# Performance work log

Measured on AMD Instinct MI355X. Metric: run time of the kernel, lower is better.

## Reference

```python
import jax, jax.numpy as jnp
import numpy as np

N = 50000   # nodes
F = 128     # v_feats
K = 128     # filters
H = 3       # multi_head
M = 10      # fixed neighbor count (hardcoded repeat(1,10,1) in source)


def setup_inputs() -> dict:
    key = jax.random.key(0)
    ks = jax.random.split(key, 10)
    vertices = jax.random.normal(ks[0], (N, F), jnp.float32)
    nh_indices = jax.random.randint(ks[1], (N, M), 0, N)
    int_indices = jax.random.randint(ks[2], (N, M), 0, N)
    nh_edges = jax.random.uniform(ks[3], (N, M), jnp.float32)
    int_edges = jax.random.uniform(ks[4], (N, M), jnp.float32)
    is_int = jax.random.randint(ks[5], (N,), 0, 2)
    scale = 0.05
    Wvc = jax.random.normal(ks[6], (H, F, K), jnp.float32) * scale
    Wvn_int = jax.random.normal(ks[7], (H, F, K), jnp.float32) * scale
    Wvn_nh = jax.random.normal(ks[8], (H, F, K), jnp.float32) * scale
    a = jax.random.normal(ks[9], (H, 2 * K, 1), jnp.float32) * scale
    bv = jnp.zeros((H, K), jnp.float32)
    return dict(vertices=vertices, nh_indices=nh_indices, int_indices=int_indices,
                nh_edges=nh_edges, int_edges=int_edges, is_int=is_int,
                Wvc=Wvc, bv=bv, Wvn_int=Wvn_int, Wvn_nh=Wvn_nh, a=a)


def reference(vertices, nh_indices, int_indices, nh_edges, int_edges, is_int,
              Wvc, bv, Wvn_int, Wvn_nh, a):
    n = vertices.shape[0]
    k = a.shape[1] // 2
    # Project center and neighbor features for all heads at once.
    Zc = jnp.einsum('nf,hfk->hnk', vertices, Wvc)        # [H,N,K]
    Vint = jnp.einsum('nf,hfk->hnk', vertices, Wvn_int)  # [H,N,K]
    Vnh = jnp.einsum('nf,hfk->hnk', vertices, Wvn_nh)    # [H,N,K]
    # cat((neighbor, center)) @ a  ==  neighbor @ a[:k] + center @ a[k:]
    a_n = a[:, :k, 0]  # [H,K]
    a_c = a[:, k:, 0]  # [H,K]
    e_center = jnp.einsum('hnk,hk->hn', Zc, a_c)[:, :, None]  # [H,N,1]

    def branch(Vside, idx, edges):
        mask = (idx != -1).astype(vertices.dtype)           # [N,M], -1 = pad
        g = Vside[:, idx]                                   # [H,N,M,K] gather
        e = jnp.einsum('hnmk,hk->hnm', g, a_n) + e_center   # [H,N,M]
        # faithful to source: scores zeroed (not -inf) by mask/edges before softmax
        e = e * mask[None] * edges[None]
        alpha = jax.nn.softmax(e, axis=2)                   # [H,N,M]
        norm = jnp.maximum(mask.sum(axis=1), 1.0)           # [N]
        Zn = jnp.einsum('hnmk,hnm->hnk', g * mask[None, :, :, None], alpha)
        return Zn / norm[None, :, None]

    Zn_inter = branch(Vint, int_indices, int_edges)
    Zn_chain = branch(Vnh, nh_indices, nh_edges)
    z = jax.nn.relu(Zc + Zn_inter + Zn_chain + bv[:, None, :])  # [H,N,K]
    # torch.cat(head outputs, dim=1) -> [N, H*K]
    return jnp.transpose(z, (1, 0, 2)).reshape(n, -1)
```

## Files before the change

kernel.cpp:

```cpp
#include <hip/hip_runtime.h>
#include <stdint.h>

#define N_V 50000
#define F_DIM 128
#define K_DIM 128
#define H_DIM 3
#define M_DIM 10

using bf16x8 = __attribute__((ext_vector_type(8))) short;
using f32x4  = __attribute__((ext_vector_type(4))) float;

__device__ inline unsigned short f2bf(float f) {
    union { float f; uint32_t u; } v; v.f = f;
    uint32_t u = v.u;
    u += 0x7fffu + ((u >> 16) & 1u);
    return (unsigned short)(u >> 16);
}

#define LDS_AS __attribute__((address_space(3)))
__device__ inline void gl2lds16(const void* g, void* l) {
    __builtin_amdgcn_global_load_lds(
        (const __attribute__((address_space(1))) unsigned int*)g,
        (LDS_AS unsigned int*)l, 16, 0, 0);
}

#define WTOT (9 * 128 * 128)
#define XCH  (N_V * 16)
#define WACT (9 * 128)

__global__ void prep(const float* __restrict__ Wvc,
                     const float* __restrict__ Wvn_int,
                     const float* __restrict__ Wvn_nh,
                     const float* __restrict__ X,
                     const float* __restrict__ a,
                     unsigned short* __restrict__ Wt,
                     unsigned short* __restrict__ Xb,
                     unsigned short* __restrict__ wab) {
    int idx = blockIdx.x * 256 + threadIdx.x;
    if (idx < WTOT) {
        int b   = idx >> 14;
        int rem = idx & 16383;
        int k = rem >> 7;
        int f = rem & 127;
        int h = b / 3, t = b - 3 * h;
        const float* src = (t == 0) ? Wvc : (t == 1) ? Wvn_int : Wvn_nh;
        Wt[idx] = f2bf(src[(h * 128 + f) * 128 + k]);
        return;
    }
    int xi = idx - WTOT;
    if (xi < XCH) {
        const float4* Xv = (const float4*)X;
        float4 v0 = Xv[xi * 2];
        float4 v1 = Xv[xi * 2 + 1];
        uint4 o;
        o.x = (uint32_t)f2bf(v0.x) | ((uint32_t)f2bf(v0.y) << 16);
        o.y = (uint32_t)f2bf(v0.z) | ((uint32_t)f2bf(v0.w) << 16);
        o.z = (uint32_t)f2bf(v1.x) | ((uint32_t)f2bf(v1.y) << 16);
        o.w = (uint32_t)f2bf(v1.z) | ((uint32_t)f2bf(v1.w) << 16);
        *(uint4*)&Xb[(size_t)xi * 8] = o;
        return;
    }
    int wi = xi - XCH;
    if (wi < WACT) {
        int b = wi >> 7, f = wi & 127;
        int h = b / 3, t = b - 3 * h;
        const float* src = (t == 0) ? Wvc : (t == 1) ? Wvn_int : Wvn_nh;
        const float4* wrow = (const float4*)&src[(h * 128 + f) * 128];
        const float4* av   = (const float4*)&a[h * 256 + (t == 0 ? 128 : 0)];
        float acc = 0.f;
        #pragma unroll 8
        for (int c = 0; c < 32; ++c) {
            float4 w = wrow[c], x = av[c];
            acc += w.x * x.x + w.y * x.y + w.z * x.z + w.w * x.w;
        }
        wab[b * 128 + f] = f2bf(acc);
    }
}

__global__ __launch_bounds__(256, 3) void gemm_kernel(
    const unsigned short* __restrict__ Xb,
    const unsigned short* __restrict__ Wt,
    const unsigned short* __restrict__ wab,
    float* __restrict__ out,
    uint8_t* __restrict__ Vint,
    uint8_t* __restrict__ Vnh,
    float* __restrict__ e_center,
    float* __restrict__ e_int,
    float* __restrict__ e_nh) {
    __shared__ unsigned short As[64 * 128];

    const int tid    = threadIdx.x;
    const int b      = blockIdx.y;
    const int h      = b / 3;
    const int t      = b - 3 * h;
    const int m_base = blockIdx.x * 64;
    const int wv     = tid >> 6;
    const int lane   = tid & 63;
    const int q      = lane >> 4;
    const int ln     = lane & 15;
    const int cb     = (wv >> 1) * 64;
    const int rb     = (wv & 1) * 32;

    const unsigned short* Wb = Wt + b * 16384;
    bf16x8 bfr[4][4];
    #pragma unroll
    for (int ct = 0; ct < 4; ++ct) {
        int col = cb + 4 * ln + ct;
        #pragma unroll
        for (int kk = 0; kk < 4; ++kk)
            bfr[ct][kk] = *(const bf16x8*)&Wb[col * 128 + kk * 32 + q * 8];
    }

    #pragma unroll
    for (int it = 0; it < 4; ++it) {
        int c16 = it * 256 + tid;
        int r   = c16 >> 4;
        int p   = c16 & 15;
        int lch = p ^ (r & 15);
        int gr  = m_base + r;
        if (gr >= N_V) gr = 0;
        gl2lds16(Xb + (size_t)gr * 128 + lch * 8, &As[c16 * 8]);
    }
    __syncthreads();

    bf16x8 afr[2][4];
    #pragma unroll
    for (int rt = 0; rt < 2; ++rt) {
        int r = rb + rt * 16 + ln;
        #pragma unroll
        for (int kk = 0; kk < 4; ++kk) {
            int p = (kk * 4 + q) ^ ln;
            afr[rt][kk] = *(const bf16x8*)&As[r * 128 + p * 8];
        }
    }

    f32x4 acc[2][4];
    #pragma unroll
    for (int rt = 0; rt < 2; ++rt)
        #pragma unroll
        for (int ct = 0; ct < 4; ++ct) acc[rt][ct] = (f32x4){0.f, 0.f, 0.f, 0.f};

    #pragma unroll
    for (int rt = 0; rt < 2; ++rt)
        #pragma unroll
        for (int kk = 0; kk < 4; ++kk)
            #pragma unroll
            for (int ct = 0; ct < 4; ++ct)
                acc[rt][ct] = __builtin_amdgcn_mfma_f32_16x16x32_bf16(
                    afr[rt][kk], bfr[ct][kk], acc[rt][ct], 0, 0, 0);

    if (wv < 2) {
        bf16x8 wz[4];
        #pragma unroll
        for (int kk = 0; kk < 4; ++kk) {
            bf16x8 z = {0, 0, 0, 0, 0, 0, 0, 0};
            if (ln == 0) z = *(const bf16x8*)&wab[b * 128 + kk * 32 + q * 8];
            wz[kk] = z;
        }
        float* e_arr = (t == 0) ? e_center : (t == 1) ? e_int : e_nh;
        #pragma unroll
        for (int rt = 0; rt < 2; ++rt) {
            f32x4 ae = (f32x4){0.f, 0.f, 0.f, 0.f};
            #pragma unroll
            for (int kk = 0; kk < 4; ++kk)
                ae = __builtin_amdgcn_mfma_f32_16x16x32_bf16(afr[rt][kk], wz[kk], ae, 0, 0, 0);
            if (ln == 0) {
                #pragma unroll
                for (int rg = 0; rg < 4; ++rg) {
                    int gr = m_base + rb + rt * 16 + q * 4 + rg;
                    if (gr < N_V) e_arr[h * N_V + gr] = ae[rg];
                }
            }
        }
    }

    const int c0 = cb + 4 * ln;
    if (t == 0) {
        #pragma unroll
        for (int rt = 0; rt < 2; ++rt)
            #pragma unroll
            for (int rg = 0; rg < 4; ++rg) {
                int gr = m_base + rb + rt * 16 + q * 4 + rg;
                if (gr >= N_V) continue;
                float4 v = make_float4(acc[rt][0][rg], acc[rt][1][rg],
                                       acc[rt][2][rg], acc[rt][3][rg]);
                *(float4*)&out[(size_t)gr * 384 + h * 128 + c0] = v;
            }
    } else {
        uint8_t* Vside = (t == 1) ? Vint : Vnh;
        #pragma unroll
        for (int rt = 0; rt < 2; ++rt)
            #pragma unroll
            for (int rg = 0; rg < 4; ++rg) {
                int gr = m_base + rb + rt * 16 + q * 4 + rg;
                if (gr >= N_V) continue;
                int pk = __builtin_amdgcn_cvt_pk_fp8_f32(
                    acc[rt][0][rg], acc[rt][1][rg], 0, false);
                pk = __builtin_amdgcn_cvt_pk_fp8_f32(
                    acc[rt][2][rg], acc[rt][3][rg], pk, true);
                *(uint32_t*)&Vside[((size_t)(h * N_V + gr)) * 128 + c0] =
                    (uint32_t)pk;
            }
    }
}

__global__ __launch_bounds__(256) void attn_head_kernel(
    const int* __restrict__ nh_idx, const int* __restrict__ int_idx,
    const float* __restrict__ nh_edge, const float* __restrict__ int_edge,
    const float* __restrict__ bv_h,
    const uint8_t* __restrict__ Vint_h,
    const uint8_t* __restrict__ Vnh_h,
    const float* __restrict__ ec_h, const float* __restrict__ ei_h,
    const float* __restrict__ en_h,
    float* __restrict__ out, int hoff) {
    const int wv   = threadIdx.x >> 6;
    const int lane = threadIdx.x & 63;
    const int n    = blockIdx.x * 4 + wv;
    if (n >= N_V) return;
    const int g  = lane >> 4;
    const int gl = lane & 15;

    const bool part = (g <= 1) && (gl < M_DIM);
    int jm = -1; float wm = 0.f;
    if (part) {
        const int*   idx = (g == 0) ? int_idx  : nh_idx;
        const float* ed  = (g == 0) ? int_edge : nh_edge;
        jm = idx[n * M_DIM + gl];
        wm = ed[n * M_DIM + gl];
    }
    const bool  valid = part && (jm >= 0);
    const int   jc    = valid ? jm : 0;
    const float vfl   = valid ? 1.f : 0.f;

    float ec = ec_h[n];

    float l = -3.0e38f;
    if (part) {
        const float* es = (g == 0) ? ei_h : en_h;
        float e = es[jc];
        l = valid ? (e + ec) * wm : 0.f;
    }
    float mx = l;
    #pragma unroll
    for (int off = 1; off < 16; off <<= 1) mx = fmaxf(mx, __shfl_xor(mx, off, 64));
    float ex = part ? __expf(l - mx) : 0.f;
    float sv = ex, cf = vfl;
    #pragma unroll
    for (int off = 1; off < 16; off <<= 1) {
        sv += __shfl_xor(sv, off, 64);
        cf += __shfl_xor(cf, off, 64);
    }
    float alphap = 0.f;
    if (valid) alphap = ex / (sv * fmaxf(cf, 1.f));

    const uint8_t* Vb = (g < 2) ? Vint_h : Vnh_h;
    const int src_base = (g < 2 ? 0 : 16) + (g & 1) * 5;
    float acc[8] = {0.f, 0.f, 0.f, 0.f, 0.f, 0.f, 0.f, 0.f};
    #pragma unroll
    for (int i = 0; i < 5; ++i) {
        int   src = src_base + i;
        int   j   = __shfl(jc, src, 64);
        float al  = __shfl(alphap, src, 64);
        uint2 pv  = *(const uint2*)&Vb[(size_t)j * 128 + gl * 8];
        auto f01 = __builtin_amdgcn_cvt_pk_f32_fp8(pv.x, false);
        auto f23 = __builtin_amdgcn_cvt_pk_f32_fp8(pv.x, true);
        auto f45 = __builtin_amdgcn_cvt_pk_f32_fp8(pv.y, false);
        auto f67 = __builtin_amdgcn_cvt_pk_f32_fp8(pv.y, true);
        acc[0] += al * f01[0];
        acc[1] += al * f01[1];
        acc[2] += al * f23[0];
        acc[3] += al * f23[1];
        acc[4] += al * f45[0];
        acc[5] += al * f45[1];
        acc[6] += al * f67[0];
        acc[7] += al * f67[1];
    }
    #pragma unroll
    for (int c = 0; c < 8; ++c) {
        acc[c] += __shfl_xor(acc[c], 16, 64);
        acc[c] += __shfl_xor(acc[c], 32, 64);
    }
    if (g < 2) {
        size_t o = (size_t)n * 384 + hoff + gl * 8 + g * 4;
        float4 zc = *(const float4*)&out[o];
        float4 bb = *(const float4*)&bv_h[gl * 8 + g * 4];
        float4 zn;
        if (g == 0) zn = make_float4(acc[0], acc[1], acc[2], acc[3]);
        else        zn = make_float4(acc[4], acc[5], acc[6], acc[7]);
        float4 r;
        r.x = fmaxf(zc.x + zn.x + bb.x, 0.f);
        r.y = fmaxf(zc.y + zn.y + bb.y, 0.f);
        r.z = fmaxf(zc.z + zn.z + bb.z, 0.f);
        r.w = fmaxf(zc.w + zn.w + bb.w, 0.f);
        *(float4*)&out[o] = r;
    }
}

extern "C" void kernel_launch(void* const* d_in, const int* in_sizes, int n_in,
                              void* d_out, int out_size, void* d_ws, size_t ws_size,
                              hipStream_t stream) {
    const float* vertices    = (const float*)d_in[0];
    const int*   nh_indices  = (const int*)d_in[1];
    const int*   int_indices = (const int*)d_in[2];
    const float* nh_edges    = (const float*)d_in[3];
    const float* int_edges   = (const float*)d_in[4];
    const float* Wvc     = (const float*)d_in[6];
    const float* bv      = (const float*)d_in[7];
    const float* Wvn_int = (const float*)d_in[8];
    const float* Wvn_nh  = (const float*)d_in[9];
    const float* a       = (const float*)d_in[10];
    float* out = (float*)d_out;

    char* ws = (char*)d_ws;
    size_t off = 0;
    unsigned short* Wt = (unsigned short*)(ws + off);
    off += (size_t)WTOT * 2;                  off = (off + 255) & ~(size_t)255;
    unsigned short* wab = (unsigned short*)(ws + off);
    off += (size_t)WACT * 2;                  off = (off + 255) & ~(size_t)255;
    unsigned short* Xb = (unsigned short*)(ws + off);
    off += (size_t)N_V * 128 * 2;             off = (off + 255) & ~(size_t)255;
    uint8_t* Vint = (uint8_t*)(ws + off);
    off += (size_t)H_DIM * N_V * 128;         off = (off + 255) & ~(size_t)255;
    uint8_t* Vnh = (uint8_t*)(ws + off);
    off += (size_t)H_DIM * N_V * 128;         off = (off + 255) & ~(size_t)255;
    float* e_center = (float*)(ws + off);
    off += (size_t)H_DIM * N_V * 4;           off = (off + 255) & ~(size_t)255;
    float* e_int = (float*)(ws + off);
    off += (size_t)H_DIM * N_V * 4;           off = (off + 255) & ~(size_t)255;
    float* e_nh = (float*)(ws + off);
    off += (size_t)H_DIM * N_V * 4;

    int prep_threads = WTOT + XCH + WACT;
    prep<<<(prep_threads + 255) / 256, 256, 0, stream>>>(
        Wvc, Wvn_int, Wvn_nh, vertices, a, Wt, Xb, wab);

    dim3 grid_g((N_V + 63) / 64, 9);
    gemm_kernel<<<grid_g, 256, 0, stream>>>(Xb, Wt, wab, out, Vint, Vnh,
                                            e_center, e_int, e_nh);

    for (int h = 0; h < H_DIM; ++h) {
        attn_head_kernel<<<(N_V + 3) / 4, 256, 0, stream>>>(
            nh_indices, int_indices, nh_edges, int_edges,
            bv + h * 128,
            Vint + (size_t)h * N_V * 128,
            Vnh  + (size_t)h * N_V * 128,
            e_center + (size_t)h * N_V,
            e_int    + (size_t)h * N_V,
            e_nh     + (size_t)h * N_V,
            out, h * 128);
    }
}
```

Measured before the change: 258.5 us.

## Loop all nine weight blocks per GEMM tile and merge per-head attention launches

The GEMM grid drops its 9-way y dimension. Each block now loads its 64-row X tile into LDS once and loops over all nine head/type weight blocks, and the nine attention-score dot products are computed in a single MFMA pass using lanes 0-8. The three per-head attention launches become one kernel that loads neighbor indices, edges and the mask count once and loops over heads. The aim is to avoid reloading X tiles and index data and to cut launch overhead. The cost is a GEMM grid with nine times fewer blocks, each doing serial work and reloading weights per iteration, which may reduce parallelism and latency hiding.

```diff
diff --git a/kernel.cpp b/kernel.cpp
--- a/kernel.cpp
+++ b/kernel.cpp
@@ -90,9 +90,6 @@
     __shared__ unsigned short As[64 * 128];
 
     const int tid    = threadIdx.x;
-    const int b      = blockIdx.y;
-    const int h      = b / 3;
-    const int t      = b - 3 * h;
     const int m_base = blockIdx.x * 64;
     const int wv     = tid >> 6;
     const int lane   = tid & 63;
@@ -100,16 +97,6 @@
     const int ln     = lane & 15;
     const int cb     = (wv >> 1) * 64;
     const int rb     = (wv & 1) * 32;
-
-    const unsigned short* Wb = Wt + b * 16384;
-    bf16x8 bfr[4][4];
-    #pragma unroll
-    for (int ct = 0; ct < 4; ++ct) {
-        int col = cb + 4 * ln + ct;
-        #pragma unroll
-        for (int kk = 0; kk < 4; ++kk)
-            bfr[ct][kk] = *(const bf16x8*)&Wb[col * 128 + kk * 32 + q * 8];
-    }
 
     #pragma unroll
     for (int it = 0; it < 4; ++it) {
@@ -134,85 +121,101 @@
         }
     }
 
-    f32x4 acc[2][4];
-    #pragma unroll
-    for (int rt = 0; rt < 2; ++rt)
-        #pragma unroll
-        for (int ct = 0; ct < 4; ++ct) acc[rt][ct] = (f32x4){0.f, 0.f, 0.f, 0.f};
-
-    #pragma unroll
-    for (int rt = 0; rt < 2; ++rt)
-        #pragma unroll
-        for (int kk = 0; kk < 4; ++kk)
-            #pragma unroll
-            for (int ct = 0; ct < 4; ++ct)
-                acc[rt][ct] = __builtin_amdgcn_mfma_f32_16x16x32_bf16(
-                    afr[rt][kk], bfr[ct][kk], acc[rt][ct], 0, 0, 0);
-
     if (wv < 2) {
         bf16x8 wz[4];
         #pragma unroll
         for (int kk = 0; kk < 4; ++kk) {
             bf16x8 z = {0, 0, 0, 0, 0, 0, 0, 0};
-            if (ln == 0) z = *(const bf16x8*)&wab[b * 128 + kk * 32 + q * 8];
+            if (ln < 9) z = *(const bf16x8*)&wab[ln * 128 + kk * 32 + q * 8];
             wz[kk] = z;
         }
-        float* e_arr = (t == 0) ? e_center : (t == 1) ? e_int : e_nh;
         #pragma unroll
         for (int rt = 0; rt < 2; ++rt) {
             f32x4 ae = (f32x4){0.f, 0.f, 0.f, 0.f};
             #pragma unroll
             for (int kk = 0; kk < 4; ++kk)
                 ae = __builtin_amdgcn_mfma_f32_16x16x32_bf16(afr[rt][kk], wz[kk], ae, 0, 0, 0);
-            if (ln == 0) {
+            if (ln < 9) {
+                int hh = ln / 3, tt = ln - 3 * hh;
+                float* ep = (tt == 0) ? e_center : (tt == 1) ? e_int : e_nh;
                 #pragma unroll
                 for (int rg = 0; rg < 4; ++rg) {
                     int gr = m_base + rb + rt * 16 + q * 4 + rg;
-                    if (gr < N_V) e_arr[h * N_V + gr] = ae[rg];
+                    if (gr < N_V) ep[hh * N_V + gr] = ae[rg];
                 }
             }
         }
     }
 
     const int c0 = cb + 4 * ln;
-    if (t == 0) {
+    #pragma unroll 1
+    for (int b = 0; b < 9; ++b) {
+        const unsigned short* Wb = Wt + (size_t)b * 16384;
+        bf16x8 bfr[4][4];
+        #pragma unroll
+        for (int ct = 0; ct < 4; ++ct) {
+            int col = cb + 4 * ln + ct;
+            #pragma unroll
+            for (int kk = 0; kk < 4; ++kk)
+                bfr[ct][kk] = *(const bf16x8*)&Wb[col * 128 + kk * 32 + q * 8];
+        }
+
+        f32x4 acc[2][4];
         #pragma unroll
         for (int rt = 0; rt < 2; ++rt)
             #pragma unroll
-            for (int rg = 0; rg < 4; ++rg) {
-                int gr = m_base + rb + rt * 16 + q * 4 + rg;
-                if (gr >= N_V) continue;
-                float4 v = make_float4(acc[rt][0][rg], acc[rt][1][rg],
-                                       acc[rt][2][rg], acc[rt][3][rg]);
-                *(float4*)&out[(size_t)gr * 384 + h * 128 + c0] = v;
-            }
-    } else {
-        uint8_t* Vside = (t == 1) ? Vint : Vnh;
+            for (int ct = 0; ct < 4; ++ct) acc[rt][ct] = (f32x4){0.f, 0.f, 0.f, 0.f};
+
         #pragma unroll
         for (int rt = 0; rt < 2; ++rt)
             #pragma unroll
-            for (int rg = 0; rg < 4; ++rg) {
-                int gr = m_base + rb + rt * 16 + q * 4 + rg;
-                if (gr >= N_V) continue;
-                int pk = __builtin_amdgcn_cvt_pk_fp8_f32(
-                    acc[rt][0][rg], acc[rt][1][rg], 0, false);
-                pk = __builtin_amdgcn_cvt_pk_fp8_f32(
-                    acc[rt][2][rg], acc[rt][3][rg], pk, true);
-                *(uint32_t*)&Vside[((size_t)(h * N_V + gr)) * 128 + c0] =
-                    (uint32_t)pk;
-            }
-    }
-}
-
-__global__ __launch_bounds__(256) void attn_head_kernel(
+            for (int kk = 0; kk < 4; ++kk)
+                #pragma unroll
+                for (int ct = 0; ct < 4; ++ct)
+                    acc[rt][ct] = __builtin_amdgcn_mfma_f32_16x16x32_bf16(
+                        afr[rt][kk], bfr[ct][kk], acc[rt][ct], 0, 0, 0);
+
+        int hh = b / 3;
+        int tt = b - 3 * hh;
+        if (tt == 0) {
+            #pragma unroll
+            for (int rt = 0; rt < 2; ++rt)
+                #pragma unroll
+                for (int rg = 0; rg < 4; ++rg) {
+                    int gr = m_base + rb + rt * 16 + q * 4 + rg;
+                    if (gr >= N_V) continue;
+                    float4 v = make_float4(acc[rt][0][rg], acc[rt][1][rg],
+                                           acc[rt][2][rg], acc[rt][3][rg]);
+                    *(float4*)&out[(size_t)gr * 384 + hh * 128 + c0] = v;
+                }
+        } else {
+            uint8_t* Vside = (tt == 1) ? Vint : Vnh;
+            #pragma unroll
+            for (int rt = 0; rt < 2; ++rt)
+                #pragma unroll
+                for (int rg = 0; rg < 4; ++rg) {
+                    int gr = m_base + rb + rt * 16 + q * 4 + rg;
+                    if (gr >= N_V) continue;
+                    int pk = __builtin_amdgcn_cvt_pk_fp8_f32(
+                        acc[rt][0][rg], acc[rt][1][rg], 0, false);
+                    pk = __builtin_amdgcn_cvt_pk_fp8_f32(
+                        acc[rt][2][rg], acc[rt][3][rg], pk, true);
+                    *(uint32_t*)&Vside[((size_t)(hh * N_V + gr)) * 128 + c0] =
+                        (uint32_t)pk;
+                }
+        }
+    }
+}
+
+__global__ __launch_bounds__(256) void attn_kernel(
     const int* __restrict__ nh_idx, const int* __restrict__ int_idx,
     const float* __restrict__ nh_edge, const float* __restrict__ int_edge,
-    const float* __restrict__ bv_h,
-    const uint8_t* __restrict__ Vint_h,
-    const uint8_t* __restrict__ Vnh_h,
-    const float* __restrict__ ec_h, const float* __restrict__ ei_h,
-    const float* __restrict__ en_h,
-    float* __restrict__ out, int hoff) {
+    const float* __restrict__ bv,
+    const uint8_t* __restrict__ Vint,
+    const uint8_t* __restrict__ Vnh,
+    const float* __restrict__ ec, const float* __restrict__ ei,
+    const float* __restrict__ en,
+    float* __restrict__ out) {
     const int wv   = threadIdx.x >> 6;
     const int lane = threadIdx.x & 63;
     const int n    = blockIdx.x * 4 + wv;
@@ -232,67 +235,72 @@
     const int   jc    = valid ? jm : 0;
     const float vfl   = valid ? 1.f : 0.f;
 
-    float ec = ec_h[n];
-
-    float l = -3.0e38f;
-    if (part) {
-        const float* es = (g == 0) ? ei_h : en_h;
-        float e = es[jc];
-        l = valid ? (e + ec) * wm : 0.f;
-    }
-    float mx = l;
+    float cf = vfl;
     #pragma unroll
-    for (int off = 1; off < 16; off <<= 1) mx = fmaxf(mx, __shfl_xor(mx, off, 64));
-    float ex = part ? __expf(l - mx) : 0.f;
-    float sv = ex, cf = vfl;
+    for (int off = 1; off < 16; off <<= 1) cf += __shfl_xor(cf, off, 64);
+    const float cnorm = fmaxf(cf, 1.f);
+
+    const int src_base = (g < 2 ? 0 : 16) + (g & 1) * 5;
+    int jrow[5];
     #pragma unroll
-    for (int off = 1; off < 16; off <<= 1) {
-        sv += __shfl_xor(sv, off, 64);
-        cf += __shfl_xor(cf, off, 64);
-    }
-    float alphap = 0.f;
-    if (valid) alphap = ex / (sv * fmaxf(cf, 1.f));
-
-    const uint8_t* Vb = (g < 2) ? Vint_h : Vnh_h;
-    const int src_base = (g < 2 ? 0 : 16) + (g & 1) * 5;
-    float acc[8] = {0.f, 0.f, 0.f, 0.f, 0.f, 0.f, 0.f, 0.f};
-    #pragma unroll
-    for (int i = 0; i < 5; ++i) {
-        int   src = src_base + i;
-        int   j   = __shfl(jc, src, 64);
-        float al  = __shfl(alphap, src, 64);
-        uint2 pv  = *(const uint2*)&Vb[(size_t)j * 128 + gl * 8];
-        auto f01 = __builtin_amdgcn_cvt_pk_f32_fp8(pv.x, false);
-        auto f23 = __builtin_amdgcn_cvt_pk_f32_fp8(pv.x, true);
-        auto f45 = __builtin_amdgcn_cvt_pk_f32_fp8(pv.y, false);
-        auto f67 = __builtin_amdgcn_cvt_pk_f32_fp8(pv.y, true);
-        acc[0] += al * f01[0];
-        acc[1] += al * f01[1];
-        acc[2] += al * f23[0];
-        acc[3] += al * f23[1];
-        acc[4] += al * f45[0];
-        acc[5] += al * f45[1];
-        acc[6] += al * f67[0];
-        acc[7] += al * f67[1];
-    }
-    #pragma unroll
-    for (int c = 0; c < 8; ++c) {
-        acc[c] += __shfl_xor(acc[c], 16, 64);
-        acc[c] += __shfl_xor(acc[c], 32, 64);
-    }
-    if (g < 2) {
-        size_t o = (size_t)n * 384 + hoff + gl * 8 + g * 4;
-        float4 zc = *(const float4*)&out[o];
-        float4 bb = *(const float4*)&bv_h[gl * 8 + g * 4];
-        float4 zn;
-        if (g == 0) zn = make_float4(acc[0], acc[1], acc[2], acc[3]);
-        else        zn = make_float4(acc[4], acc[5], acc[6], acc[7]);
-        float4 r;
-        r.x = fmaxf(zc.x + zn.x + bb.x, 0.f);
-        r.y = fmaxf(zc.y + zn.y + bb.y, 0.f);
-        r.z = fmaxf(zc.z + zn.z + bb.z, 0.f);
-        r.w = fmaxf(zc.w + zn.w + bb.w, 0.f);
-        *(float4*)&out[o] = r;
+    for (int i = 0; i < 5; ++i) jrow[i] = __shfl(jc, src_base + i, 64);
+
+    for (int h = 0; h < H_DIM; ++h) {
+        const float ecv = ec[h * N_V + n];
+
+        float l = -3.0e38f;
+        if (part) {
+            const float* es = (g == 0) ? ei : en;
+            float e = es[h * N_V + jc];
+            l = valid ? (e + ecv) * wm : 0.f;
+        }
+        float mx = l;
+        #pragma unroll
+        for (int off = 1; off < 16; off <<= 1) mx = fmaxf(mx, __shfl_xor(mx, off, 64));
+        float ex = part ? __expf(l - mx) : 0.f;
+        float sv = ex;
+        #pragma unroll
+        for (int off = 1; off < 16; off <<= 1) sv += __shfl_xor(sv, off, 64);
+        float alphap = valid ? ex / (sv * cnorm) : 0.f;
+
+        const uint8_t* Vb = ((g < 2) ? Vint : Vnh) + (size_t)h * N_V * 128;
+        float acc[8] = {0.f, 0.f, 0.f, 0.f, 0.f, 0.f, 0.f, 0.f};
+        #pragma unroll
+        for (int i = 0; i < 5; ++i) {
+            float al  = __shfl(alphap, src_base + i, 64);
+            uint2 pv  = *(const uint2*)&Vb[(size_t)jrow[i] * 128 + gl * 8];
+            auto f01 = __builtin_amdgcn_cvt_pk_f32_fp8(pv.x, false);
+            auto f23 = __builtin_amdgcn_cvt_pk_f32_fp8(pv.x, true);
+            auto f45 = __builtin_amdgcn_cvt_pk_f32_fp8(pv.y, false);
+            auto f67 = __builtin_amdgcn_cvt_pk_f32_fp8(pv.y, true);
+            acc[0] += al * f01[0];
+            acc[1] += al * f01[1];
+            acc[2] += al * f23[0];
+            acc[3] += al * f23[1];
+            acc[4] += al * f45[0];
+            acc[5] += al * f45[1];
+            acc[6] += al * f67[0];
+            acc[7] += al * f67[1];
+        }
+        #pragma unroll
+        for (int c = 0; c < 8; ++c) {
+            acc[c] += __shfl_xor(acc[c], 16, 64);
+            acc[c] += __shfl_xor(acc[c], 32, 64);
+        }
+        if (g < 2) {
+            size_t o = (size_t)n * 384 + h * 128 + gl * 8 + g * 4;
+            float4 zc = *(const float4*)&out[o];
+            float4 bb = *(const float4*)&bv[h * 128 + gl * 8 + g * 4];
+            float4 zn;
+            if (g == 0) zn = make_float4(acc[0], acc[1], acc[2], acc[3]);
+            else        zn = make_float4(acc[4], acc[5], acc[6], acc[7]);
+            float4 r;
+            r.x = fmaxf(zc.x + zn.x + bb.x, 0.f);
+            r.y = fmaxf(zc.y + zn.y + bb.y, 0.f);
+            r.z = fmaxf(zc.z + zn.z + bb.z, 0.f);
+            r.w = fmaxf(zc.w + zn.w + bb.w, 0.f);
+            *(float4*)&out[o] = r;
+        }
     }
 }
 
@@ -334,19 +342,11 @@
     prep<<<(prep_threads + 255) / 256, 256, 0, stream>>>(
         Wvc, Wvn_int, Wvn_nh, vertices, a, Wt, Xb, wab);
 
-    dim3 grid_g((N_V + 63) / 64, 9);
+    dim3 grid_g((N_V + 63) / 64);
     gemm_kernel<<<grid_g, 256, 0, stream>>>(Xb, Wt, wab, out, Vint, Vnh,
                                             e_center, e_int, e_nh);
 
-    for (int h = 0; h < H_DIM; ++h) {
-        attn_head_kernel<<<(N_V + 3) / 4, 256, 0, stream>>>(
-            nh_indices, int_indices, nh_edges, int_edges,
-            bv + h * 128,
-            Vint + (size_t)h * N_V * 128,
-            Vnh  + (size_t)h * N_V * 128,
-            e_center + (size_t)h * N_V,
-            e_int    + (size_t)h * N_V,
-            e_nh     + (size_t)h * N_V,
-            out, h * 128);
-    }
-}
+    attn_kernel<<<(N_V + 3) / 4, 256, 0, stream>>>(
+        nh_indices, int_indices, nh_edges, int_edges, bv,
+        Vint, Vnh, e_center, e_int, e_nh, out);
+}
```

Measured after the change: 275.4 us. 1.07x slower.
